# Performance work log

Measured on AMD Instinct MI355X. Metric: run time of the kernel, lower is better.

## Reference

```python
import jax, jax.numpy as jnp
import numpy as np

# Production-scale 3D conv: B=4, C=64->64, 32^3 volume, 3x3x3 kernel, stride 1, pad 1.
B, CIN, COUT = 4, 64, 64
KSIZE = (3, 3, 3)
STRIDE = (1, 1, 1)
PAD = 1
SPATIAL = (32, 32, 32)


def setup_inputs() -> dict:
    key = jax.random.key(0)
    k1, k2, k3 = jax.random.split(key, 3)
    x = jax.random.normal(k1, (B, CIN) + SPATIAL, dtype=jnp.float32)
    weight = jax.random.normal(k2, (COUT, CIN) + KSIZE, dtype=jnp.float32)
    bias = jax.random.normal(k3, (COUT,), dtype=jnp.float32)
    return {"x": x, "weight": weight, "bias": bias}


def reference(x, weight, bias):
    # The original materializes all sliding-window patches via nested unfold and
    # contracts with einsum('bci...,oci->bo...'). That is exactly a standard
    # cross-correlation (torch-style conv). We express the same math as a direct
    # convolution, avoiding the O(kernel_volume) patch blowup.
    out = jax.lax.conv_general_dilated(
        x,
        weight,
        window_strides=STRIDE,
        padding=[(PAD, PAD)] * 3,
        dimension_numbers=("NCDHW", "OIDHW", "NCDHW"),
    )
    return out + bias.reshape(1, -1, 1, 1, 1)
```

## Files before the change

### kernel.cpp

```cpp
#include <hip/hip_runtime.h>
#include <hip/hip_bf16.h>

#define WS_W_OFF    0
#define WS_ZERO_OFF 221184
#define WS_XT_OFF   262144

typedef __attribute__((ext_vector_type(8))) short s16x8;
typedef __attribute__((ext_vector_type(4))) float f32x4;

#define GLOBAL_AS __attribute__((address_space(1)))
#define LDS_AS    __attribute__((address_space(3)))

__device__ __forceinline__ unsigned short f2bf(float f) {
  unsigned u = __builtin_bit_cast(unsigned, f);
  u = u + 0x7fffu + ((u >> 16) & 1u);
  return (unsigned short)(u >> 16);
}

__global__ void prep_kernel(const float* __restrict__ x,
                            const float* __restrict__ w,
                            unsigned short* __restrict__ wsw,
                            float* __restrict__ zeros,
                            unsigned short* __restrict__ xt) {
  int blk = blockIdx.x;
  if (blk < 432) {
    int t = blk * 256 + threadIdx.x;
    int tap  = t % 27;
    int cin  = (t / 27) & 63;
    int cout = t / (27 * 64);
    int st2 = cin >> 5;
    int q   = (cin >> 3) & 3;
    int j   = cin & 7;
    int nf  = cout >> 4;
    int lane = q * 16 + (cout & 15);
    int dst = (((tap * 2 + st2) * 4 + nf) * 64 + lane) * 8 + j;
    wsw[dst] = f2bf(w[t]);
    if (t < 64) zeros[t] = 0.0f;
  } else {
    int t  = (blk - 432) * 256 + threadIdx.x;
    int s  = t & 32767;
    int c8 = (t >> 15) & 7;
    int b  = t >> 18;
    const float* src = x + (size_t)(b * 64 + c8 * 8) * 32768 + s;
    s16x8 v;
    #pragma unroll
    for (int k = 0; k < 8; ++k) v[k] = (short)f2bf(src[(size_t)k * 32768]);
    *(s16x8*)(xt + (size_t)(b * 32768 + s) * 64 + c8 * 8) = v;
  }
}

__global__ __launch_bounds__(256, 4) void conv_kernel(const float* __restrict__ bias,
                                                      float* __restrict__ out,
                                                      const char* __restrict__ ws) {
  __shared__ unsigned char halo[39 * 1024];

  const int tid  = threadIdx.x;
  const int lane = tid & 63;
  const int w    = tid >> 6;
  const int logical = (blockIdx.x & 7) * 128 + (blockIdx.x >> 3);
  const int yt = logical & 7, z = (logical >> 3) & 31, b = logical >> 8;
  const int y0 = yt * 4;

  const int r15 = lane & 15;
  const int hi4 = lane >> 4;

  const int sl_sub  = lane >> 2;
  const int sl_slot = (lane & 3) ^ ((lane >> 4) & 3);

  auto stage = [&](int h) {
    for (int g = w; g < 39; g += 4) {
      int pos = g * 16 + sl_sub;
      int hz = pos / 204; int rem = pos - hz * 204;
      int hy = rem / 34;  int hx = rem - hy * 34;
      int gz = z + hz - 1, gy = y0 + hy - 1, gx = hx - 1;
      bool inb = (pos < 612) & ((unsigned)gz < 32u) &
                 ((unsigned)gy < 32u) & ((unsigned)gx < 32u);
      int s = (gz * 32 + gy) * 32 + gx;
      int src = inb ? (WS_XT_OFF + (b * 32768 + s) * 128 + h * 64 + sl_slot * 16)
                    : WS_ZERO_OFF;
      __builtin_amdgcn_global_load_lds(
          (const GLOBAL_AS void*)(ws + src),
          (LDS_AS void*)(&halo[g * 1024 + lane * 16]),
          16, 0, 0);
    }
  };

  const s16x8* __restrict__ wfr = (const s16x8*)(ws + WS_W_OFF);

  f32x4 zero4 = {0.f, 0.f, 0.f, 0.f};
  f32x4 acc[2][4];
  #pragma unroll
  for (int mf = 0; mf < 2; ++mf)
    #pragma unroll
    for (int nf = 0; nf < 4; ++nf) acc[mf][nf] = zero4;

  s16x8 BA[4], BB[4];

  auto loadB = [&](s16x8* dst, int h, int tap) {
    #pragma unroll
    for (int nf = 0; nf < 4; ++nf)
      dst[nf] = wfr[((tap * 2 + h) * 4 + nf) * 64 + lane];
  };

  auto compute = [&](int tap, const s16x8* B) {
    int kd = tap / 9; int rem9 = tap - kd * 9;
    int kh = rem9 / 3; int kw = rem9 - kh * 3;
    int prow = (kd * 6 + w + kh) * 34 + r15 + kw;
    s16x8 a[2];
    #pragma unroll
    for (int mf = 0; mf < 2; ++mf) {
      int pos  = prow + mf * 16;
      int addr = ((pos >> 4) << 10) | ((pos & 15) << 6)
               | ((hi4 ^ ((pos >> 2) & 3)) << 4);
      a[mf] = *(const s16x8*)&halo[addr];
    }
    #pragma unroll
    for (int mf = 0; mf < 2; ++mf)
      #pragma unroll
      for (int nf = 0; nf < 4; ++nf)
        acc[mf][nf] = __builtin_amdgcn_mfma_f32_16x16x32_bf16(
            a[mf], B[nf], acc[mf][nf], 0, 0, 0);
  };

  stage(0);
  loadB(BA, 0, 0);
  __syncthreads();
  for (int t = 0; t < 13; ++t) {
    loadB(BB, 0, 2 * t + 1); compute(2 * t, BA);
    loadB(BA, 0, 2 * t + 2); compute(2 * t + 1, BB);
  }
  compute(26, BA);

  loadB(BA, 1, 0);
  __syncthreads();
  stage(1);
  __syncthreads();
  for (int t = 0; t < 13; ++t) {
    loadB(BB, 1, 2 * t + 1); compute(2 * t, BA);
    loadB(BA, 1, 2 * t + 2); compute(2 * t + 1, BB);
  }
  compute(26, BA);

  const int y = y0 + w;
  #pragma unroll
  for (int nf = 0; nf < 4; ++nf) {
    int cout = nf * 16 + r15;
    float bv = bias[cout];
    float* orow = out + ((size_t)((b * 64 + cout) * 32 + z) * 32 + y) * 32;
    #pragma unroll
    for (int mf = 0; mf < 2; ++mf) {
      int x0 = mf * 16 + 4 * hi4;
      f32x4 v;
      #pragma unroll
      for (int r = 0; r < 4; ++r) v[r] = acc[mf][nf][r] + bv;
      *(f32x4*)&orow[x0] = v;
    }
  }
}

extern "C" void kernel_launch(void* const* d_in, const int* in_sizes, int n_in,
                              void* d_out, int out_size, void* d_ws, size_t ws_size,
                              hipStream_t stream) {
  const float* x    = (const float*)d_in[0];
  const float* wgt  = (const float*)d_in[1];
  const float* bias = (const float*)d_in[2];
  float* out = (float*)d_out;
  char* ws = (char*)d_ws;

  prep_kernel<<<4528, 256, 0, stream>>>(x, wgt,
                                        (unsigned short*)(ws + WS_W_OFF),
                                        (float*)(ws + WS_ZERO_OFF),
                                        (unsigned short*)(ws + WS_XT_OFF));
  conv_kernel<<<1024, 256, 0, stream>>>(bias, out, ws);
}
```

Measured before the change: 54.66 us.

## Use 2-wave blocks with 2 output rows per wave and prefetch A fragments

Result: faster. 49.07 us (-10.2%).

```diff
diff --git a/kernel.cpp b/kernel.cpp
--- a/kernel.cpp
+++ b/kernel.cpp
@@ -28,12 +28,12 @@
     int tap  = t % 27;
     int cin  = (t / 27) & 63;
     int cout = t / (27 * 64);
-    int st2 = cin >> 5;
+    int h   = cin >> 5;
     int q   = (cin >> 3) & 3;
     int j   = cin & 7;
     int nf  = cout >> 4;
     int lane = q * 16 + (cout & 15);
-    int dst = (((tap * 2 + st2) * 4 + nf) * 64 + lane) * 8 + j;
+    int dst = (((tap * 2 + h) * 4 + nf) * 64 + lane) * 8 + j;
     wsw[dst] = f2bf(w[t]);
     if (t < 64) zeros[t] = 0.0f;
   } else {
@@ -49,7 +49,7 @@
   }
 }
 
-__global__ __launch_bounds__(256, 4) void conv_kernel(const float* __restrict__ bias,
+__global__ __launch_bounds__(128, 2) void conv_kernel(const float* __restrict__ bias,
                                                       float* __restrict__ out,
                                                       const char* __restrict__ ws) {
   __shared__ unsigned char halo[39 * 1024];
@@ -64,11 +64,11 @@
   const int r15 = lane & 15;
   const int hi4 = lane >> 4;
 
-  const int sl_sub  = lane >> 2;
-  const int sl_slot = (lane & 3) ^ ((lane >> 4) & 3);
+  const int sl_sub   = lane >> 2;
+  const int sl_chunk = lane & 3;
 
   auto stage = [&](int h) {
-    for (int g = w; g < 39; g += 4) {
+    for (int g = w; g < 39; g += 2) {
       int pos = g * 16 + sl_sub;
       int hz = pos / 204; int rem = pos - hz * 204;
       int hy = rem / 34;  int hx = rem - hy * 34;
@@ -76,7 +76,7 @@
       bool inb = (pos < 612) & ((unsigned)gz < 32u) &
                  ((unsigned)gy < 32u) & ((unsigned)gx < 32u);
       int s = (gz * 32 + gy) * 32 + gx;
-      int src = inb ? (WS_XT_OFF + (b * 32768 + s) * 128 + h * 64 + sl_slot * 16)
+      int src = inb ? (WS_XT_OFF + (b * 32768 + s) * 128 + h * 64 + sl_chunk * 16)
                     : WS_ZERO_OFF;
       __builtin_amdgcn_global_load_lds(
           (const GLOBAL_AS void*)(ws + src),
@@ -88,13 +88,13 @@
   const s16x8* __restrict__ wfr = (const s16x8*)(ws + WS_W_OFF);
 
   f32x4 zero4 = {0.f, 0.f, 0.f, 0.f};
-  f32x4 acc[2][4];
+  f32x4 acc[4][4];
   #pragma unroll
-  for (int mf = 0; mf < 2; ++mf)
+  for (int mf = 0; mf < 4; ++mf)
     #pragma unroll
     for (int nf = 0; nf < 4; ++nf) acc[mf][nf] = zero4;
 
-  s16x8 BA[4], BB[4];
+  s16x8 B0[4], B1[4], A0[4], A1[4];
 
   auto loadB = [&](s16x8* dst, int h, int tap) {
     #pragma unroll
@@ -102,54 +102,49 @@
       dst[nf] = wfr[((tap * 2 + h) * 4 + nf) * 64 + lane];
   };
 
-  auto compute = [&](int tap, const s16x8* B) {
-    int kd = tap / 9; int rem9 = tap - kd * 9;
-    int kh = rem9 / 3; int kw = rem9 - kh * 3;
-    int prow = (kd * 6 + w + kh) * 34 + r15 + kw;
-    s16x8 a[2];
+  auto loadA = [&](s16x8* a, int tap) {
+    int kd = tap / 9; int r9 = tap - kd * 9;
+    int kh = r9 / 3;  int kw = r9 - kh * 3;
+    int prow = (kd * 6 + 2 * w + kh) * 34 + kw + r15;
     #pragma unroll
-    for (int mf = 0; mf < 2; ++mf) {
-      int pos  = prow + mf * 16;
-      int addr = ((pos >> 4) << 10) | ((pos & 15) << 6)
-               | ((hi4 ^ ((pos >> 2) & 3)) << 4);
-      a[mf] = *(const s16x8*)&halo[addr];
+    for (int mf = 0; mf < 4; ++mf) {
+      int pos = prow + (mf >> 1) * 34 + (mf & 1) * 16;
+      a[mf] = *(const s16x8*)&halo[pos * 64 + hi4 * 16];
     }
+  };
+
+  auto compute = [&](const s16x8* a, const s16x8* B) {
     #pragma unroll
-    for (int mf = 0; mf < 2; ++mf)
+    for (int mf = 0; mf < 4; ++mf)
       #pragma unroll
       for (int nf = 0; nf < 4; ++nf)
         acc[mf][nf] = __builtin_amdgcn_mfma_f32_16x16x32_bf16(
             a[mf], B[nf], acc[mf][nf], 0, 0, 0);
   };
 
-  stage(0);
-  loadB(BA, 0, 0);
-  __syncthreads();
-  for (int t = 0; t < 13; ++t) {
-    loadB(BB, 0, 2 * t + 1); compute(2 * t, BA);
-    loadB(BA, 0, 2 * t + 2); compute(2 * t + 1, BB);
+  #pragma unroll 1
+  for (int h = 0; h < 2; ++h) {
+    if (h) __syncthreads();
+    stage(h);
+    loadB(B0, h, 0);
+    __syncthreads();
+    loadA(A0, 0);
+    for (int t = 0; t < 13; ++t) {
+      loadB(B1, h, 2 * t + 1); loadA(A1, 2 * t + 1); compute(A0, B0);
+      loadB(B0, h, 2 * t + 2); loadA(A0, 2 * t + 2); compute(A1, B1);
+    }
+    compute(A0, B0);
   }
-  compute(26, BA);
 
-  loadB(BA, 1, 0);
-  __syncthreads();
-  stage(1);
-  __syncthreads();
-  for (int t = 0; t < 13; ++t) {
-    loadB(BB, 1, 2 * t + 1); compute(2 * t, BA);
-    loadB(BA, 1, 2 * t + 2); compute(2 * t + 1, BB);
-  }
-  compute(26, BA);
-
-  const int y = y0 + w;
   #pragma unroll
   for (int nf = 0; nf < 4; ++nf) {
     int cout = nf * 16 + r15;
     float bv = bias[cout];
-    float* orow = out + ((size_t)((b * 64 + cout) * 32 + z) * 32 + y) * 32;
     #pragma unroll
-    for (int mf = 0; mf < 2; ++mf) {
-      int x0 = mf * 16 + 4 * hi4;
+    for (int mf = 0; mf < 4; ++mf) {
+      int y  = y0 + 2 * w + (mf >> 1);
+      int x0 = (mf & 1) * 16 + 4 * hi4;
+      float* orow = out + ((size_t)((b * 64 + cout) * 32 + z) * 32 + y) * 32;
       f32x4 v;
       #pragma unroll
       for (int r = 0; r < 4; ++r) v[r] = acc[mf][nf][r] + bv;
@@ -171,5 +166,5 @@
                                         (unsigned short*)(ws + WS_W_OFF),
                                         (float*)(ws + WS_ZERO_OFF),
                                         (unsigned short*)(ws + WS_XT_OFF));
-  conv_kernel<<<1024, 256, 0, stream>>>(bias, out, ws);
+  conv_kernel<<<1024, 128, 0, stream>>>(bias, out, ws);
 }
```
